# Optimization experiments

Measured on AMD Instinct MI355X. Metric: run time of the kernel, lower is better.

## Reference

```python
import jax, jax.numpy as jnp
import numpy as np

N_ATOMS = 25000
MAX_NBR = 32
D = 128


def setup_inputs() -> dict:
    key = jax.random.key(0)
    ks = jax.random.split(key, 12)
    s1 = 1.0 / np.sqrt(2 * D)
    s2 = 1.0 / np.sqrt(D)
    return {
        "atom_features": jax.random.normal(ks[0], (N_ATOMS, D), dtype=jnp.float32),
        "nbr_features": jax.random.normal(ks[1], (N_ATOMS, MAX_NBR, D), dtype=jnp.float32),
        "nbr_indices": jax.random.randint(ks[2], (N_ATOMS, MAX_NBR), 0, N_ATOMS, dtype=jnp.int64),
        # message_net: Linear(2D->D), ReLU, Linear(D->D)
        "msg_W1": jax.random.uniform(ks[3], (2 * D, D), jnp.float32, -s1, s1),
        "msg_b1": jax.random.uniform(ks[4], (D,), jnp.float32, -s1, s1),
        "msg_W2": jax.random.uniform(ks[5], (D, D), jnp.float32, -s2, s2),
        "msg_b2": jax.random.uniform(ks[6], (D,), jnp.float32, -s2, s2),
        # update_net: Linear(2D->D), ReLU, Linear(D->D)
        "upd_W1": jax.random.uniform(ks[7], (2 * D, D), jnp.float32, -s1, s1),
        "upd_b1": jax.random.uniform(ks[8], (D,), jnp.float32, -s1, s1),
        "upd_W2": jax.random.uniform(ks[9], (D, D), jnp.float32, -s2, s2),
        "upd_b2": jax.random.uniform(ks[10], (D,), jnp.float32, -s2, s2),
    }


def reference(atom_features, nbr_features, nbr_indices,
              msg_W1, msg_b1, msg_W2, msg_b2,
              upd_W1, upd_b1, upd_W2, upd_b2):
    # NOTE: nbr_features is accepted but unused, matching the original forward.
    N, M = nbr_indices.shape
    # gather neighbor atom features: [N, M, D]
    nbr_atom = atom_features[nbr_indices]
    # expand self features and concat: [N, M, 2D]
    self_exp = jnp.broadcast_to(atom_features[:, None, :], (N, M, atom_features.shape[-1]))
    combined = jnp.concatenate([self_exp, nbr_atom], axis=-1)
    # message MLP (per-edge)
    h = jax.nn.relu(jnp.einsum('nmf,fd->nmd', combined, msg_W1) + msg_b1)
    messages = jnp.einsum('nmd,de->nme', h, msg_W2) + msg_b2
    # sum-aggregate over neighbors: [N, D]
    agg = jnp.sum(messages, axis=1)
    # update MLP
    upd_in = jnp.concatenate([atom_features, agg], axis=-1)
    u = jax.nn.relu(upd_in @ upd_W1 + upd_b1)
    updated = u @ upd_W2 + upd_b2
    return jax.nn.relu(atom_features + updated)
```

## Files before the change

### kernel.cpp

```cpp
#include <hip/hip_runtime.h>


#define N_ATOMS 25000
#define DDIM    128
#define MNBR    32
#define RT      16
#define NROWB   1563

typedef _Float16 half8  __attribute__((ext_vector_type(8)));
typedef _Float16 half4v __attribute__((ext_vector_type(4)));
typedef float    f32x4  __attribute__((ext_vector_type(4)));

__global__ void k_detect(const int* __restrict__ idx, int* __restrict__ flag) {
  if (threadIdx.x == 0) {
    int allOddZero = 1;
    for (int w = 1; w < 64; w += 2)
      if (idx[w] != 0) { allOddZero = 0; break; }
    *flag = allOddZero;
  }
}

__global__ void k_cvt(const float* __restrict__ A, _Float16* __restrict__ Af) {
  int i = (blockIdx.x * 256 + threadIdx.x) * 4;
  f32x4 v = *reinterpret_cast<const f32x4*>(A + i);
  half4v o;
  o[0] = (_Float16)v[0]; o[1] = (_Float16)v[1];
  o[2] = (_Float16)v[2]; o[3] = (_Float16)v[3];
  *reinterpret_cast<half4v*>(Af + i) = o;
}

__global__ void k_pack(const float* __restrict__ msgW1,
                       const float* __restrict__ msgW2,
                       const float* __restrict__ updW1,
                       const float* __restrict__ updW2,
                       const float* __restrict__ msgb2,
                       const float* __restrict__ updb1,
                       _Float16* __restrict__ pw, float* __restrict__ cvec) {
  int b = blockIdx.x;
  int lane = threadIdx.x;
  if (b == 160) {
    for (int rep = 0; rep < 2; rep++) {
      int j = lane + rep * 64;
      float acc = 0.f;
      for (int e = 0; e < 128; e++)
        acc += msgb2[e] * updW1[(128 + e) * 128 + j];
      cvec[j] = 32.0f * acc + updb1[j];
    }
    return;
  }
  int mat = b >> 5;
  int t = b & 31;
  int kt = t >> 3, nt = t & 7;
  int n = nt * 16 + (lane & 15);
  int kbase = kt * 32 + (lane >> 4) * 8;
  half8 hv;
  for (int j = 0; j < 8; j++) {
    int k = kbase + j;
    float v;
    if (mat == 0)      v = msgW1[k * 128 + n];
    else if (mat == 1) v = msgW1[(128 + k) * 128 + n];
    else if (mat == 2) v = updW1[k * 128 + n];
    else if (mat == 4) v = updW2[k * 128 + n];
    else {
      float acc = 0.f;
      for (int e = 0; e < 128; e++)
        acc += msgW2[k * 128 + e] * updW1[(128 + e) * 128 + n];
      v = acc;
    }
    hv[j] = (_Float16)v;
  }
  *reinterpret_cast<half8*>(pw + (size_t)mat * 16384 + ((size_t)(kt * 8 + nt) * 64 + lane) * 8) = hv;
}

__global__ __launch_bounds__(256) void k_stp(const _Float16* __restrict__ Af,
                                             const _Float16* __restrict__ pw,
                                             const float* __restrict__ msgb1,
                                             _Float16* __restrict__ S,
                                             _Float16* __restrict__ T,
                                             _Float16* __restrict__ P) {
  int r0 = blockIdx.x * RT;
  int mat = blockIdx.y;
  int wave = threadIdx.x >> 6, lane = threadIdx.x & 63;
  int m16 = lane & 15, q = lane >> 4;
  const _Float16* pwm = pw + (size_t)mat * 16384;
  _Float16* outp = (mat == 0) ? S : (mat == 1) ? T : P;

  int arow = r0 + m16; if (arow > N_ATOMS - 1) arow = N_ATOMS - 1;
  f32x4 acc0 = {0.f, 0.f, 0.f, 0.f}, acc1 = {0.f, 0.f, 0.f, 0.f};
  int nt0 = wave, nt1 = wave + 4;
  for (int kt = 0; kt < 4; kt++) {
    half8 a  = *reinterpret_cast<const half8*>(Af + (size_t)arow * DDIM + kt * 32 + q * 8);
    half8 b0 = *reinterpret_cast<const half8*>(pwm + ((size_t)(kt * 8 + nt0) * 64 + lane) * 8);
    half8 b1 = *reinterpret_cast<const half8*>(pwm + ((size_t)(kt * 8 + nt1) * 64 + lane) * 8);
    acc0 = __builtin_amdgcn_mfma_f32_16x16x32_f16(a, b0, acc0, 0, 0, 0);
    acc1 = __builtin_amdgcn_mfma_f32_16x16x32_f16(a, b1, acc1, 0, 0, 0);
  }
  for (int h = 0; h < 2; h++) {
    f32x4 acc = h ? acc1 : acc0;
    int nt = h ? nt1 : nt0;
    int col = nt * 16 + m16;
    float bias = (mat == 0) ? msgb1[col] : 0.0f;
    for (int reg = 0; reg < 4; reg++) {
      int row = r0 + q * 4 + reg;
      if (row < N_ATOMS)
        outp[(size_t)row * DDIM + col] = (_Float16)(acc[reg] + bias);
    }
  }
}

__global__ void k_gather(const _Float16* __restrict__ S, const _Float16* __restrict__ T,
                         const int* __restrict__ idx, const int* __restrict__ flag64,
                         _Float16* __restrict__ Hsum) {
  int lane32 = threadIdx.x & 31;
  int atom = blockIdx.x * 8 + (threadIdx.x >> 5);
  int c = lane32 * 4;
  bool w64 = (*flag64 != 0);
  const half4v s = *reinterpret_cast<const half4v*>(S + (size_t)atom * DDIM + c);
  float s0 = (float)s[0], s1 = (float)s[1], s2 = (float)s[2], s3 = (float)s[3];
  float a0 = 0.f, a1 = 0.f, a2 = 0.f, a3 = 0.f;
  const int* ip = idx + (w64 ? (size_t)atom * MNBR * 2 : (size_t)atom * MNBR);
  int stride = w64 ? 2 : 1;
#pragma unroll 8
  for (int m = 0; m < MNBR; m++) {
    int j = ip[m * stride];
    const half4v t = *reinterpret_cast<const half4v*>(T + (size_t)j * DDIM + c);
    float v0 = s0 + (float)t[0]; a0 += fmaxf(v0, 0.f);
    float v1 = s1 + (float)t[1]; a1 += fmaxf(v1, 0.f);
    float v2 = s2 + (float)t[2]; a2 += fmaxf(v2, 0.f);
    float v3 = s3 + (float)t[3]; a3 += fmaxf(v3, 0.f);
  }
  half4v o; o[0] = (_Float16)a0; o[1] = (_Float16)a1; o[2] = (_Float16)a2; o[3] = (_Float16)a3;
  *reinterpret_cast<half4v*>(Hsum + (size_t)atom * DDIM + c) = o;
}

__global__ __launch_bounds__(256) void k_upd(const _Float16* __restrict__ Hsum,
                                             const _Float16* __restrict__ P,
                                             const _Float16* __restrict__ pw,
                                             const float* __restrict__ cvec,
                                             const float* __restrict__ A,
                                             const float* __restrict__ updb2,
                                             float* __restrict__ out) {
  __shared__ __align__(16) _Float16 u_lds[16][136];
  int r0 = blockIdx.x * RT;
  int wave = threadIdx.x >> 6, lane = threadIdx.x & 63;
  int m16 = lane & 15, q = lane >> 4;
  const _Float16* pwu = pw + (size_t)3 * 16384;
  const _Float16* pw2 = pw + (size_t)4 * 16384;
  int arow = r0 + m16; if (arow > N_ATOMS - 1) arow = N_ATOMS - 1;

  for (int h = 0; h < 2; h++) {
    int nt = wave + h * 4;
    f32x4 acc = {0.f, 0.f, 0.f, 0.f};
    for (int kt = 0; kt < 4; kt++) {
      half8 a = *reinterpret_cast<const half8*>(Hsum + (size_t)arow * DDIM + kt * 32 + q * 8);
      half8 b = *reinterpret_cast<const half8*>(pwu + ((size_t)(kt * 8 + nt) * 64 + lane) * 8);
      acc = __builtin_amdgcn_mfma_f32_16x16x32_f16(a, b, acc, 0, 0, 0);
    }
    int col = nt * 16 + m16;
    float cv = cvec[col];
    for (int reg = 0; reg < 4; reg++) {
      int rowl = q * 4 + reg;
      int row = r0 + rowl;
      int prow = row < N_ATOMS ? row : N_ATOMS - 1;
      float u = (float)P[(size_t)prow * DDIM + col] + acc[reg] + cv;
      u_lds[rowl][col] = (_Float16)(u > 0.f ? u : 0.f);
    }
  }
  __syncthreads();

  for (int h = 0; h < 2; h++) {
    int nt = wave + h * 4;
    f32x4 acc = {0.f, 0.f, 0.f, 0.f};
    for (int kt = 0; kt < 4; kt++) {
      half8 a = *reinterpret_cast<const half8*>(&u_lds[m16][kt * 32 + q * 8]);
      half8 b = *reinterpret_cast<const half8*>(pw2 + ((size_t)(kt * 8 + nt) * 64 + lane) * 8);
      acc = __builtin_amdgcn_mfma_f32_16x16x32_f16(a, b, acc, 0, 0, 0);
    }
    int col = nt * 16 + m16;
    float b2v = updb2[col];
    for (int reg = 0; reg < 4; reg++) {
      int row = r0 + q * 4 + reg;
      if (row < N_ATOMS) {
        float v = A[(size_t)row * DDIM + col] + acc[reg] + b2v;
        out[(size_t)row * DDIM + col] = (v > 0.f ? v : 0.f);
      }
    }
  }
}

extern "C" void kernel_launch(void* const* d_in, const int* in_sizes, int n_in,
                              void* d_out, int out_size, void* d_ws, size_t ws_size,
                              hipStream_t stream) {
  const float* A      = (const float*)d_in[0];
  const int*   nbrIdx = (const int*)d_in[2];
  const float* msgW1  = (const float*)d_in[3];
  const float* msgb1  = (const float*)d_in[4];
  const float* msgW2  = (const float*)d_in[5];
  const float* msgb2  = (const float*)d_in[6];
  const float* updW1  = (const float*)d_in[7];
  const float* updb1  = (const float*)d_in[8];
  const float* updW2  = (const float*)d_in[9];
  const float* updb2  = (const float*)d_in[10];
  float* out = (float*)d_out;

  char* ws = (char*)d_ws;
  _Float16* Af   = (_Float16*)(ws);
  _Float16* S    = (_Float16*)(ws + 6400000);
  _Float16* T    = (_Float16*)(ws + 12800000);
  _Float16* P    = (_Float16*)(ws + 19200000);
  _Float16* Hs   = (_Float16*)(ws + 25600000);
  _Float16* pw   = (_Float16*)(ws + 32000000);
  float*    cvec = (float*)   (ws + 32163840);
  int*      flag = (int*)     (ws + 32164352);

  k_detect<<<1, 64, 0, stream>>>(nbrIdx, flag);
  k_cvt   <<<3125, 256, 0, stream>>>(A, Af);
  k_pack  <<<161, 64, 0, stream>>>(msgW1, msgW2, updW1, updW2, msgb2, updb1, pw, cvec);
  k_stp   <<<dim3(NROWB, 3), 256, 0, stream>>>(Af, pw, msgb1, S, T, P);
  k_gather<<<3125, 256, 0, stream>>>(S, T, nbrIdx, flag, Hs);
  k_upd   <<<NROWB, 256, 0, stream>>>(Hs, P, pw, cvec, A, updb2, out);
}
```

Baseline: 541.7 us.

## Fuse gather into update kernel, drop fp16 conversion and P intermediate

Measured after the change: 524.5 us. 3.2% less time.

```diff
diff --git a/kernel.cpp b/kernel.cpp
--- a/kernel.cpp
+++ b/kernel.cpp
@@ -4,7 +4,6 @@
 #define N_ATOMS 25000
 #define DDIM    128
 #define MNBR    32
-#define RT      16
 #define NROWB   1563
 
 typedef _Float16 half8  __attribute__((ext_vector_type(8)));
@@ -12,21 +11,9 @@
 typedef float    f32x4  __attribute__((ext_vector_type(4)));
 
 __global__ void k_detect(const int* __restrict__ idx, int* __restrict__ flag) {
-  if (threadIdx.x == 0) {
-    int allOddZero = 1;
-    for (int w = 1; w < 64; w += 2)
-      if (idx[w] != 0) { allOddZero = 0; break; }
-    *flag = allOddZero;
-  }
-}
-
-__global__ void k_cvt(const float* __restrict__ A, _Float16* __restrict__ Af) {
-  int i = (blockIdx.x * 256 + threadIdx.x) * 4;
-  f32x4 v = *reinterpret_cast<const f32x4*>(A + i);
-  half4v o;
-  o[0] = (_Float16)v[0]; o[1] = (_Float16)v[1];
-  o[2] = (_Float16)v[2]; o[3] = (_Float16)v[3];
-  *reinterpret_cast<half4v*>(Af + i) = o;
+  int v = idx[threadIdx.x * 2 + 1];
+  unsigned long long b = __ballot(v != 0);
+  if (threadIdx.x == 0) *flag = (b == 0ULL) ? 1 : 0;
 }
 
 __global__ void k_pack(const float* __restrict__ msgW1,
@@ -54,116 +41,151 @@
   int n = nt * 16 + (lane & 15);
   int kbase = kt * 32 + (lane >> 4) * 8;
   half8 hv;
-  for (int j = 0; j < 8; j++) {
-    int k = kbase + j;
-    float v;
-    if (mat == 0)      v = msgW1[k * 128 + n];
-    else if (mat == 1) v = msgW1[(128 + k) * 128 + n];
-    else if (mat == 2) v = updW1[k * 128 + n];
-    else if (mat == 4) v = updW2[k * 128 + n];
-    else {
-      float acc = 0.f;
-      for (int e = 0; e < 128; e++)
-        acc += msgW2[k * 128 + e] * updW1[(128 + e) * 128 + n];
-      v = acc;
-    }
-    hv[j] = (_Float16)v;
+  if (mat == 3) {
+    float acc[8] = {0.f, 0.f, 0.f, 0.f, 0.f, 0.f, 0.f, 0.f};
+    for (int e = 0; e < 128; e++) {
+      float w = updW1[(128 + e) * 128 + n];
+#pragma unroll
+      for (int j = 0; j < 8; j++)
+        acc[j] += msgW2[(kbase + j) * 128 + e] * w;
+    }
+#pragma unroll
+    for (int j = 0; j < 8; j++) hv[j] = (_Float16)acc[j];
+  } else {
+    const float* src = (mat == 0) ? msgW1
+                     : (mat == 1) ? (msgW1 + 128 * 128)
+                     : (mat == 2) ? updW1 : updW2;
+#pragma unroll
+    for (int j = 0; j < 8; j++) hv[j] = (_Float16)src[(kbase + j) * 128 + n];
   }
   *reinterpret_cast<half8*>(pw + (size_t)mat * 16384 + ((size_t)(kt * 8 + nt) * 64 + lane) * 8) = hv;
 }
 
-__global__ __launch_bounds__(256) void k_stp(const _Float16* __restrict__ Af,
-                                             const _Float16* __restrict__ pw,
-                                             const float* __restrict__ msgb1,
-                                             _Float16* __restrict__ S,
-                                             _Float16* __restrict__ T,
-                                             _Float16* __restrict__ P) {
-  int r0 = blockIdx.x * RT;
-  int mat = blockIdx.y;
+__global__ __launch_bounds__(256) void k_st(const float* __restrict__ A,
+                                            const _Float16* __restrict__ pw,
+                                            const float* __restrict__ msgb1,
+                                            _Float16* __restrict__ S,
+                                            _Float16* __restrict__ T) {
+  int r0 = blockIdx.x * 16;
   int wave = threadIdx.x >> 6, lane = threadIdx.x & 63;
   int m16 = lane & 15, q = lane >> 4;
-  const _Float16* pwm = pw + (size_t)mat * 16384;
-  _Float16* outp = (mat == 0) ? S : (mat == 1) ? T : P;
-
+  const _Float16* pw0 = pw;
+  const _Float16* pw1 = pw + 16384;
   int arow = r0 + m16; if (arow > N_ATOMS - 1) arow = N_ATOMS - 1;
-  f32x4 acc0 = {0.f, 0.f, 0.f, 0.f}, acc1 = {0.f, 0.f, 0.f, 0.f};
+
+  f32x4 aS0 = {0,0,0,0}, aS1 = {0,0,0,0}, aT0 = {0,0,0,0}, aT1 = {0,0,0,0};
   int nt0 = wave, nt1 = wave + 4;
   for (int kt = 0; kt < 4; kt++) {
-    half8 a  = *reinterpret_cast<const half8*>(Af + (size_t)arow * DDIM + kt * 32 + q * 8);
-    half8 b0 = *reinterpret_cast<const half8*>(pwm + ((size_t)(kt * 8 + nt0) * 64 + lane) * 8);
-    half8 b1 = *reinterpret_cast<const half8*>(pwm + ((size_t)(kt * 8 + nt1) * 64 + lane) * 8);
-    acc0 = __builtin_amdgcn_mfma_f32_16x16x32_f16(a, b0, acc0, 0, 0, 0);
-    acc1 = __builtin_amdgcn_mfma_f32_16x16x32_f16(a, b1, acc1, 0, 0, 0);
+    const float* ap = A + (size_t)arow * DDIM + kt * 32 + q * 8;
+    f32x4 lo = *reinterpret_cast<const f32x4*>(ap);
+    f32x4 hi = *reinterpret_cast<const f32x4*>(ap + 4);
+    half8 a;
+    a[0]=(_Float16)lo[0]; a[1]=(_Float16)lo[1]; a[2]=(_Float16)lo[2]; a[3]=(_Float16)lo[3];
+    a[4]=(_Float16)hi[0]; a[5]=(_Float16)hi[1]; a[6]=(_Float16)hi[2]; a[7]=(_Float16)hi[3];
+    half8 bS0 = *reinterpret_cast<const half8*>(pw0 + ((size_t)(kt * 8 + nt0) * 64 + lane) * 8);
+    half8 bS1 = *reinterpret_cast<const half8*>(pw0 + ((size_t)(kt * 8 + nt1) * 64 + lane) * 8);
+    half8 bT0 = *reinterpret_cast<const half8*>(pw1 + ((size_t)(kt * 8 + nt0) * 64 + lane) * 8);
+    half8 bT1 = *reinterpret_cast<const half8*>(pw1 + ((size_t)(kt * 8 + nt1) * 64 + lane) * 8);
+    aS0 = __builtin_amdgcn_mfma_f32_16x16x32_f16(a, bS0, aS0, 0, 0, 0);
+    aS1 = __builtin_amdgcn_mfma_f32_16x16x32_f16(a, bS1, aS1, 0, 0, 0);
+    aT0 = __builtin_amdgcn_mfma_f32_16x16x32_f16(a, bT0, aT0, 0, 0, 0);
+    aT1 = __builtin_amdgcn_mfma_f32_16x16x32_f16(a, bT1, aT1, 0, 0, 0);
   }
   for (int h = 0; h < 2; h++) {
-    f32x4 acc = h ? acc1 : acc0;
     int nt = h ? nt1 : nt0;
     int col = nt * 16 + m16;
-    float bias = (mat == 0) ? msgb1[col] : 0.0f;
+    f32x4 as = h ? aS1 : aS0;
+    f32x4 at = h ? aT1 : aT0;
+    float bias = msgb1[col];
     for (int reg = 0; reg < 4; reg++) {
       int row = r0 + q * 4 + reg;
-      if (row < N_ATOMS)
-        outp[(size_t)row * DDIM + col] = (_Float16)(acc[reg] + bias);
-    }
-  }
-}
-
-__global__ void k_gather(const _Float16* __restrict__ S, const _Float16* __restrict__ T,
-                         const int* __restrict__ idx, const int* __restrict__ flag64,
-                         _Float16* __restrict__ Hsum) {
-  int lane32 = threadIdx.x & 31;
-  int atom = blockIdx.x * 8 + (threadIdx.x >> 5);
-  int c = lane32 * 4;
-  bool w64 = (*flag64 != 0);
-  const half4v s = *reinterpret_cast<const half4v*>(S + (size_t)atom * DDIM + c);
-  float s0 = (float)s[0], s1 = (float)s[1], s2 = (float)s[2], s3 = (float)s[3];
-  float a0 = 0.f, a1 = 0.f, a2 = 0.f, a3 = 0.f;
-  const int* ip = idx + (w64 ? (size_t)atom * MNBR * 2 : (size_t)atom * MNBR);
-  int stride = w64 ? 2 : 1;
+      if (row < N_ATOMS) {
+        S[(size_t)row * DDIM + col] = (_Float16)(as[reg] + bias);
+        T[(size_t)row * DDIM + col] = (_Float16)(at[reg]);
+      }
+    }
+  }
+}
+
+__global__ __launch_bounds__(256) void k_gupd(const _Float16* __restrict__ S,
+                                              const _Float16* __restrict__ T,
+                                              const int* __restrict__ idx,
+                                              const int* __restrict__ flag64,
+                                              const _Float16* __restrict__ pw,
+                                              const float* __restrict__ cvec,
+                                              const float* __restrict__ A,
+                                              const float* __restrict__ updb2,
+                                              float* __restrict__ out) {
+  __shared__ __align__(16) _Float16 hs[16][136];
+  __shared__ __align__(16) _Float16 ul[16][136];
+  int r0 = blockIdx.x * 16;
+  int tid = threadIdx.x;
+
+  {
+    int rowl = tid >> 4;
+    int c = (tid & 15) * 8;
+    int a = r0 + rowl; if (a > N_ATOMS - 1) a = N_ATOMS - 1;
+    bool w64 = (*flag64 != 0);
+    half8 s = *reinterpret_cast<const half8*>(S + (size_t)a * DDIM + c);
+    float ac[8] = {0.f,0.f,0.f,0.f,0.f,0.f,0.f,0.f};
+    const int* ip = idx + (w64 ? (size_t)a * MNBR * 2 : (size_t)a * MNBR);
+    int stride = w64 ? 2 : 1;
 #pragma unroll 8
-  for (int m = 0; m < MNBR; m++) {
-    int j = ip[m * stride];
-    const half4v t = *reinterpret_cast<const half4v*>(T + (size_t)j * DDIM + c);
-    float v0 = s0 + (float)t[0]; a0 += fmaxf(v0, 0.f);
-    float v1 = s1 + (float)t[1]; a1 += fmaxf(v1, 0.f);
-    float v2 = s2 + (float)t[2]; a2 += fmaxf(v2, 0.f);
-    float v3 = s3 + (float)t[3]; a3 += fmaxf(v3, 0.f);
-  }
-  half4v o; o[0] = (_Float16)a0; o[1] = (_Float16)a1; o[2] = (_Float16)a2; o[3] = (_Float16)a3;
-  *reinterpret_cast<half4v*>(Hsum + (size_t)atom * DDIM + c) = o;
-}
-
-__global__ __launch_bounds__(256) void k_upd(const _Float16* __restrict__ Hsum,
-                                             const _Float16* __restrict__ P,
-                                             const _Float16* __restrict__ pw,
-                                             const float* __restrict__ cvec,
-                                             const float* __restrict__ A,
-                                             const float* __restrict__ updb2,
-                                             float* __restrict__ out) {
-  __shared__ __align__(16) _Float16 u_lds[16][136];
-  int r0 = blockIdx.x * RT;
-  int wave = threadIdx.x >> 6, lane = threadIdx.x & 63;
+    for (int m = 0; m < MNBR; m++) {
+      int j = ip[m * stride];
+      half8 t = *reinterpret_cast<const half8*>(T + (size_t)j * DDIM + c);
+#pragma unroll
+      for (int e = 0; e < 8; e++) {
+        float v = (float)s[e] + (float)t[e];
+        ac[e] += fmaxf(v, 0.f);
+      }
+    }
+    half8 o;
+#pragma unroll
+    for (int e = 0; e < 8; e++) o[e] = (_Float16)ac[e];
+    *reinterpret_cast<half8*>(&hs[rowl][c]) = o;
+  }
+  __syncthreads();
+
+  int wave = tid >> 6, lane = tid & 63;
   int m16 = lane & 15, q = lane >> 4;
+  const _Float16* pwp = pw + (size_t)2 * 16384;
   const _Float16* pwu = pw + (size_t)3 * 16384;
   const _Float16* pw2 = pw + (size_t)4 * 16384;
   int arow = r0 + m16; if (arow > N_ATOMS - 1) arow = N_ATOMS - 1;
 
+  half8 hf[4], af[4];
+#pragma unroll
+  for (int kt = 0; kt < 4; kt++) {
+    hf[kt] = *reinterpret_cast<const half8*>(&hs[m16][kt * 32 + q * 8]);
+    const float* ap = A + (size_t)arow * DDIM + kt * 32 + q * 8;
+    f32x4 lo = *reinterpret_cast<const f32x4*>(ap);
+    f32x4 hi = *reinterpret_cast<const f32x4*>(ap + 4);
+    half8 a;
+    a[0]=(_Float16)lo[0]; a[1]=(_Float16)lo[1]; a[2]=(_Float16)lo[2]; a[3]=(_Float16)lo[3];
+    a[4]=(_Float16)hi[0]; a[5]=(_Float16)hi[1]; a[6]=(_Float16)hi[2]; a[7]=(_Float16)hi[3];
+    af[kt] = a;
+  }
+
   for (int h = 0; h < 2; h++) {
     int nt = wave + h * 4;
     f32x4 acc = {0.f, 0.f, 0.f, 0.f};
+#pragma unroll
     for (int kt = 0; kt < 4; kt++) {
-      half8 a = *reinterpret_cast<const half8*>(Hsum + (size_t)arow * DDIM + kt * 32 + q * 8);
-      half8 b = *reinterpret_cast<const half8*>(pwu + ((size_t)(kt * 8 + nt) * 64 + lane) * 8);
-      acc = __builtin_amdgcn_mfma_f32_16x16x32_f16(a, b, acc, 0, 0, 0);
+      half8 bu = *reinterpret_cast<const half8*>(pwu + ((size_t)(kt * 8 + nt) * 64 + lane) * 8);
+      acc = __builtin_amdgcn_mfma_f32_16x16x32_f16(hf[kt], bu, acc, 0, 0, 0);
+    }
+#pragma unroll
+    for (int kt = 0; kt < 4; kt++) {
+      half8 bp = *reinterpret_cast<const half8*>(pwp + ((size_t)(kt * 8 + nt) * 64 + lane) * 8);
+      acc = __builtin_amdgcn_mfma_f32_16x16x32_f16(af[kt], bp, acc, 0, 0, 0);
     }
     int col = nt * 16 + m16;
     float cv = cvec[col];
     for (int reg = 0; reg < 4; reg++) {
       int rowl = q * 4 + reg;
-      int row = r0 + rowl;
-      int prow = row < N_ATOMS ? row : N_ATOMS - 1;
-      float u = (float)P[(size_t)prow * DDIM + col] + acc[reg] + cv;
-      u_lds[rowl][col] = (_Float16)(u > 0.f ? u : 0.f);
+      float u = acc[reg] + cv;
+      ul[rowl][col] = (_Float16)(u > 0.f ? u : 0.f);
     }
   }
   __syncthreads();
@@ -171,8 +193,9 @@
   for (int h = 0; h < 2; h++) {
     int nt = wave + h * 4;
     f32x4 acc = {0.f, 0.f, 0.f, 0.f};
+#pragma unroll
     for (int kt = 0; kt < 4; kt++) {
-      half8 a = *reinterpret_cast<const half8*>(&u_lds[m16][kt * 32 + q * 8]);
+      half8 a = *reinterpret_cast<const half8*>(&ul[m16][kt * 32 + q * 8]);
       half8 b = *reinterpret_cast<const half8*>(pw2 + ((size_t)(kt * 8 + nt) * 64 + lane) * 8);
       acc = __builtin_amdgcn_mfma_f32_16x16x32_f16(a, b, acc, 0, 0, 0);
     }
@@ -204,19 +227,14 @@
   float* out = (float*)d_out;
 
   char* ws = (char*)d_ws;
-  _Float16* Af   = (_Float16*)(ws);
-  _Float16* S    = (_Float16*)(ws + 6400000);
-  _Float16* T    = (_Float16*)(ws + 12800000);
-  _Float16* P    = (_Float16*)(ws + 19200000);
-  _Float16* Hs   = (_Float16*)(ws + 25600000);
-  _Float16* pw   = (_Float16*)(ws + 32000000);
-  float*    cvec = (float*)   (ws + 32163840);
-  int*      flag = (int*)     (ws + 32164352);
+  _Float16* S    = (_Float16*)(ws);
+  _Float16* T    = (_Float16*)(ws + 6400000);
+  _Float16* pw   = (_Float16*)(ws + 12800000);
+  float*    cvec = (float*)   (ws + 12963840);
+  int*      flag = (int*)     (ws + 12964352);
 
   k_detect<<<1, 64, 0, stream>>>(nbrIdx, flag);
-  k_cvt   <<<3125, 256, 0, stream>>>(A, Af);
   k_pack  <<<161, 64, 0, stream>>>(msgW1, msgW2, updW1, updW2, msgb2, updb1, pw, cvec);
-  k_stp   <<<dim3(NROWB, 3), 256, 0, stream>>>(Af, pw, msgb1, S, T, P);
-  k_gather<<<3125, 256, 0, stream>>>(S, T, nbrIdx, flag, Hs);
-  k_upd   <<<NROWB, 256, 0, stream>>>(Hs, P, pw, cvec, A, updb2, out);
-}
+  k_st    <<<NROWB, 256, 0, stream>>>(A, pw, msgb1, S, T);
+  k_gupd  <<<NROWB, 256, 0, stream>>>(S, T, nbrIdx, flag, pw, cvec, A, updb2, out);
+}
```
